# Optimization experiments

Measured on AMD Instinct MI355X. Metric: run time of the kernel, lower is better.

## Reference

```python
import jax, jax.numpy as jnp
import numpy as np

D_MODEL = 1024
NHEADS = 16
DK = D_MODEL // NHEADS  # 64
B, LQ, LK = 4, 1024, 1024


def setup_inputs() -> dict:
    key = jax.random.key(0)
    ks = jax.random.split(key, 5)
    q = jax.random.normal(ks[0], (B, LQ, NHEADS, DK), dtype=jnp.float32)
    k = jax.random.normal(ks[1], (B, LK, NHEADS, DK), dtype=jnp.float32)
    v = jax.random.normal(ks[2], (B, LK, NHEADS, DK), dtype=jnp.float32)
    # LazyLinear materializes with in_features = LK * NHEADS due to the
    # source bug (it projects the reshaped raw score tensor, not attn@V).
    fc_w = jax.random.normal(ks[3], (D_MODEL, LK * NHEADS), dtype=jnp.float32) * 0.02
    fc_b = jax.random.normal(ks[4], (D_MODEL,), dtype=jnp.float32) * 0.02
    return {"q": q, "k": k, "v": v, "fc_w": fc_w, "fc_b": fc_b}


def reference(q, k, v, fc_w, fc_b):
    # Raw scaled scores: [b, i, j, n]
    scores = jnp.einsum('bink,bjnk->bijn', q, k) / np.float32(np.sqrt(DK))
    # NOTE (faithful to source): the softmax(dim=1) and the attn@V einsum are
    # computed in the original but their result is discarded; the output is
    # built from the raw scores. v does not influence the output.
    b, i = scores.shape[0], scores.shape[1]
    out = scores.reshape(b, i, -1)            # [b, i, j*n]
    out = out @ fc_w.T + fc_b                 # Linear(j*n -> d_model)
    return out
```

## Files before the change

### kernel.cpp

```cpp
#include <hip/hip_runtime.h>
#include <hip/hip_bf16.h>


typedef unsigned short u16;
typedef unsigned int u32;
typedef __bf16 bf16x8 __attribute__((ext_vector_type(8)));
typedef float f32x4 __attribute__((ext_vector_type(4)));
typedef u16 u16x8 __attribute__((ext_vector_type(8)));

__device__ __forceinline__ u16 f2bf(float f) {
  union { float f; unsigned u; } in;
  in.f = f;
  unsigned u = in.u;
  u += 0x7fffu + ((u >> 16) & 1u);
  return (u16)(u >> 16);
}

__global__ __launch_bounds__(256) void prep(const float* __restrict__ k,
                                            const float* __restrict__ w,
                                            u16* __restrict__ Kt,
                                            u16* __restrict__ Wt) {
  __shared__ u16 lds[16 * 520];
  const int tid = threadIdx.x;
  const int bid = blockIdx.x;

  if (bid < 1024) {
    int jt = bid & 15, n = (bid >> 4) & 15, b = bid >> 8;
    auto l2 = reinterpret_cast<u16(*)[65]>(lds);
    const int j0 = jt * 64;
    float4 r[4];
#pragma unroll
    for (int it = 0; it < 4; ++it) {
      int idx = it * 256 + tid;
      int jj = idx >> 4;
      int c4 = idx & 15;
      r[it] = *reinterpret_cast<const float4*>(
          &k[(((size_t)b * 1024 + j0 + jj) * 16 + n) * 64 + c4 * 4]);
    }
#pragma unroll
    for (int it = 0; it < 4; ++it) {
      int idx = it * 256 + tid;
      int jj = idx >> 4;
      int c4 = idx & 15;
      l2[c4 * 4 + 0][jj] = f2bf(r[it].x);
      l2[c4 * 4 + 1][jj] = f2bf(r[it].y);
      l2[c4 * 4 + 2][jj] = f2bf(r[it].z);
      l2[c4 * 4 + 3][jj] = f2bf(r[it].w);
    }
    __syncthreads();
    ushort4 o[4];
#pragma unroll
    for (int it = 0; it < 4; ++it) {
      int idx = it * 256 + tid;
      int kk = idx >> 4;
      int c4 = idx & 15;
      o[it].x = l2[kk][c4 * 4 + 0]; o[it].y = l2[kk][c4 * 4 + 1];
      o[it].z = l2[kk][c4 * 4 + 2]; o[it].w = l2[kk][c4 * 4 + 3];
    }
#pragma unroll
    for (int it = 0; it < 4; ++it) {
      int idx = it * 256 + tid;
      int kk = idx >> 4;
      int c4 = idx & 15;
      *reinterpret_cast<ushort4*>(
          &Kt[((size_t)n * 256 + b * 64 + kk) * 1024 + j0 + c4 * 4]) = o[it];
    }
  } else {
    int e = bid - 1024;
    const int d = e >> 1;
    const int h = e & 1;
    u32* lds32 = reinterpret_cast<u32*>(lds);
    const float* src = w + (size_t)d * 16384 + h * 8192;

    float4 ra[4], rb[4];
    const int gbase = ((tid >> 2) << 3) + (tid & 3);
#pragma unroll
    for (int it = 0; it < 4; ++it) {
      int g1 = it * 512 + gbase;
      ra[it] = reinterpret_cast<const float4*>(src)[g1];
      rb[it] = reinterpret_cast<const float4*>(src)[g1 + 4];
    }
    const int n0 = (tid & 3) * 4;
#pragma unroll
    for (int it = 0; it < 4; ++it) {
      int a = (it * 512 + gbase) >> 2;
#pragma unroll
      for (int el = 0; el < 4; ++el) {
        float lo = (&ra[it].x)[el], hi = (&rb[it].x)[el];
        lds32[(n0 + el) * 260 + (a >> 1)] = (u32)f2bf(lo) | ((u32)f2bf(hi) << 16);
      }
    }
    __syncthreads();
    const int wv = tid >> 6, lane = tid & 63;
    u16x8 o[4];
#pragma unroll
    for (int s = 0; s < 4; ++s)
      o[s] = *reinterpret_cast<const u16x8*>(&lds[(4 * wv + s) * 520 + lane * 8]);
#pragma unroll
    for (int s = 0; s < 4; ++s) {
      int n = 4 * wv + s;
      *reinterpret_cast<u16x8*>(
          &Wt[(size_t)n * 1048576 + (size_t)d * 1024 + h * 512 + lane * 8]) = o[s];
    }
  }
}

template <int VM>
__device__ __forceinline__ void waitVm() {
  if constexpr (VM == 16) asm volatile("s_waitcnt vmcnt(16)" ::: "memory");
  else if constexpr (VM == 8) asm volatile("s_waitcnt vmcnt(8)" ::: "memory");
  else asm volatile("s_waitcnt vmcnt(0)" ::: "memory");
}

template <int TN_TILES, int STAGE>
__global__ __launch_bounds__(256, 1) void gemm_bt(const u16* __restrict__ Abase,
                                                  const u16* __restrict__ Bbase,
                                                  u16* __restrict__ CoutBf,
                                                  float* __restrict__ CoutF,
                                                  const float* __restrict__ bias,
                                                  const float* __restrict__ qsrc,
                                                  u16* __restrict__ qdst) {
  __shared__ u16 AB[4][2][128 * 64];
  const int tid = threadIdx.x;
  const int wid = tid >> 6;
  const int lane = tid & 63;
  const int batch = blockIdx.y;
  const int tm = blockIdx.x / TN_TILES;
  const int tn = blockIdx.x % TN_TILES;

  const u16* A = Abase + (size_t)batch * 1048576;
  const u16* B = Bbase + (size_t)batch * ((STAGE == 1) ? 262144 : 1048576);
  const int row0A = tm * 128, row0B = tn * 128;

  const int wr = wid >> 1;
  const int wc = wid & 1;
  const int laneRow = lane & 15;
  const int hi8 = (lane >> 4) * 8;
  const int swz = (lane & 7) * 8;

  f32x4 acc[4][4] = {};

  auto stage = [&](int tIdx) {
    const int kt = tIdx * 64;
    u16* lA = &AB[tIdx & 3][0][0];
    u16* lB = &AB[tIdx & 3][1][0];
#pragma unroll
    for (int i = 0; i < 4; ++i) {
      int p = i * 256 + tid;
      int r = p >> 3;
      int sc = ((p & 7) ^ (r & 7)) * 8;
      const u16* gA = A + (size_t)(row0A + r) * 1024 + kt + sc;
      const u16* gB = B + (size_t)(row0B + r) * 1024 + kt + sc;
      __builtin_amdgcn_global_load_lds(
          (const __attribute__((address_space(1))) void*)gA,
          (__attribute__((address_space(3))) void*)(lA + i * 2048 + wid * 512), 16, 0, 0);
      __builtin_amdgcn_global_load_lds(
          (const __attribute__((address_space(1))) void*)gB,
          (__attribute__((address_space(3))) void*)(lB + i * 2048 + wid * 512), 16, 0, 0);
    }
  };

  auto compute = [&](int tIdx) {
    const u16* At = &AB[tIdx & 3][0][0];
    const u16* Bt = &AB[tIdx & 3][1][0];
    bf16x8 af[2][4], bq[2][4];
#pragma unroll
    for (int kh = 0; kh < 2; ++kh) {
      int cs = (kh * 32 + hi8) ^ swz;
#pragma unroll
      for (int mi = 0; mi < 4; ++mi)
        af[kh][mi] = *reinterpret_cast<const bf16x8*>(
            &At[(wr * 64 + mi * 16 + laneRow) * 64 + cs]);
#pragma unroll
      for (int ni = 0; ni < 4; ++ni)
        bq[kh][ni] = *reinterpret_cast<const bf16x8*>(
            &Bt[(wc * 64 + ni * 16 + laneRow) * 64 + cs]);
    }
#pragma unroll
    for (int kh = 0; kh < 2; ++kh)
#pragma unroll
      for (int mi = 0; mi < 4; ++mi)
#pragma unroll
        for (int ni = 0; ni < 4; ++ni)
          acc[mi][ni] = __builtin_amdgcn_mfma_f32_16x16x32_bf16(
              af[kh][mi], bq[kh][ni], acc[mi][ni], 0, 0, 0);
  };

  stage(0); stage(1); stage(2);

  for (int t = 0; t < 13; ++t) {
    waitVm<16>();
    __builtin_amdgcn_s_barrier();
    stage(t + 3);
    compute(t);
  }
  waitVm<16>(); __builtin_amdgcn_s_barrier(); compute(13);
  waitVm<8>();  __builtin_amdgcn_s_barrier(); compute(14);
  waitVm<0>();  __builtin_amdgcn_s_barrier(); compute(15);

#pragma unroll
  for (int mi = 0; mi < 4; ++mi) {
#pragma unroll
    for (int ni = 0; ni < 4; ++ni) {
      int colg = tn * 128 + wc * 64 + ni * 16 + laneRow;
#pragma unroll
      for (int qq = 0; qq < 4; ++qq) {
        int rowg = tm * 128 + wr * 64 + mi * 16 + (lane >> 4) * 4 + qq;
        if (STAGE == 1) {
          size_t off = (size_t)(colg >> 6) * 1048576 + (size_t)rowg * 1024 +
                       (size_t)batch * 64 + (colg & 63);
          CoutBf[off] = f2bf(acc[mi][ni][qq]);
        } else {
          CoutF[(size_t)batch * 1048576 + (size_t)rowg * 1024 + colg] =
              acc[mi][ni][qq] * 0.125f + bias[colg];
        }
      }
    }
  }

  if (STAGE == 1) {
    const int cb = batch * 16 + blockIdx.x;
    const float4* src = reinterpret_cast<const float4*>(qsrc) + (size_t)cb * 4096;
    ushort4* dst = reinterpret_cast<ushort4*>(qdst) + (size_t)cb * 4096;
#pragma unroll
    for (int rnd = 0; rnd < 4; ++rnd) {
      float4 r[4];
#pragma unroll
      for (int i = 0; i < 4; ++i) r[i] = src[rnd * 1024 + i * 256 + tid];
#pragma unroll
      for (int i = 0; i < 4; ++i) {
        ushort4 o;
        o.x = f2bf(r[i].x); o.y = f2bf(r[i].y);
        o.z = f2bf(r[i].z); o.w = f2bf(r[i].w);
        dst[rnd * 1024 + i * 256 + tid] = o;
      }
    }
  }
}

extern "C" void kernel_launch(void* const* d_in, const int* in_sizes, int n_in,
                              void* d_out, int out_size, void* d_ws, size_t ws_size,
                              hipStream_t stream) {
  const float* q    = (const float*)d_in[0];
  const float* k    = (const float*)d_in[1];
  const float* fc_w = (const float*)d_in[3];
  const float* fc_b = (const float*)d_in[4];
  float* out = (float*)d_out;

  char* ws = (char*)d_ws;
  if (ws_size < 58720256) return;
  u16* Qb  = (u16*)(ws);
  u16* Kt  = (u16*)(ws + 8388608);
  u16* Wt  = (u16*)(ws + 16777216);
  u16* T2t = (u16*)(ws + 50331648);

  prep<<<3072, 256, 0, stream>>>(k, fc_w, Kt, Wt);
  gemm_bt<2, 1><<<dim3(16, 16), 256, 0, stream>>>(Wt, Kt, T2t, nullptr, nullptr, q, Qb);
  gemm_bt<8, 2><<<dim3(64, 4), 256, 0, stream>>>(Qb, T2t, nullptr, out, fc_b, nullptr, nullptr);
}
```

Baseline: 60.57 us.

## Fuse fc_w fp32-to-bf16 transpose into first GEMM's A-tile loading

Removes the separate pass that converted and transposed the 64MB fc_w into a bf16 Wt workspace. The first GEMM now reads fp32 weights directly, converts them in registers with packed bf16 conversion, and writes swizzled A tiles into LDS, using a double-buffered register-prefetch pipeline. The grid is reorganised so each block handles four heads, one per wave. This avoids writing and re-reading the 32MB bf16 weight copy, at the cost of more register pressure and a simpler two-stage pipeline in the first GEMM.

```diff
diff --git a/kernel.cpp b/kernel.cpp
--- a/kernel.cpp
+++ b/kernel.cpp
@@ -6,7 +6,6 @@
 typedef unsigned int u32;
 typedef __bf16 bf16x8 __attribute__((ext_vector_type(8)));
 typedef float f32x4 __attribute__((ext_vector_type(4)));
-typedef u16 u16x8 __attribute__((ext_vector_type(8)));
 
 __device__ __forceinline__ u16 f2bf(float f) {
   union { float f; unsigned u; } in;
@@ -16,91 +15,199 @@
   return (u16)(u >> 16);
 }
 
-__global__ __launch_bounds__(256) void prep(const float* __restrict__ k,
-                                            const float* __restrict__ w,
-                                            u16* __restrict__ Kt,
-                                            u16* __restrict__ Wt) {
-  __shared__ u16 lds[16 * 520];
+__device__ __forceinline__ u32 cvt_pk_bf16(float lo, float hi) {
+  u32 r;
+  asm("v_cvt_pk_bf16_f32 %0, %1, %2" : "=v"(r) : "v"(lo), "v"(hi));
+  return r;
+}
+
+__global__ __launch_bounds__(256) void prep_k(const float* __restrict__ k,
+                                              u16* __restrict__ Kt) {
+  __shared__ u16 lds[64][65];
   const int tid = threadIdx.x;
   const int bid = blockIdx.x;
-
-  if (bid < 1024) {
-    int jt = bid & 15, n = (bid >> 4) & 15, b = bid >> 8;
-    auto l2 = reinterpret_cast<u16(*)[65]>(lds);
-    const int j0 = jt * 64;
+  int jt = bid & 15, n = (bid >> 4) & 15, b = bid >> 8;
+  const int j0 = jt * 64;
+  float4 r[4];
+#pragma unroll
+  for (int it = 0; it < 4; ++it) {
+    int idx = it * 256 + tid;
+    int jj = idx >> 4;
+    int c4 = idx & 15;
+    r[it] = *reinterpret_cast<const float4*>(
+        &k[(((size_t)b * 1024 + j0 + jj) * 16 + n) * 64 + c4 * 4]);
+  }
+#pragma unroll
+  for (int it = 0; it < 4; ++it) {
+    int idx = it * 256 + tid;
+    int jj = idx >> 4;
+    int c4 = idx & 15;
+    lds[c4 * 4 + 0][jj] = f2bf(r[it].x);
+    lds[c4 * 4 + 1][jj] = f2bf(r[it].y);
+    lds[c4 * 4 + 2][jj] = f2bf(r[it].z);
+    lds[c4 * 4 + 3][jj] = f2bf(r[it].w);
+  }
+  __syncthreads();
+  ushort4 o[4];
+#pragma unroll
+  for (int it = 0; it < 4; ++it) {
+    int idx = it * 256 + tid;
+    int kk = idx >> 4;
+    int c4 = idx & 15;
+    o[it].x = lds[kk][c4 * 4 + 0]; o[it].y = lds[kk][c4 * 4 + 1];
+    o[it].z = lds[kk][c4 * 4 + 2]; o[it].w = lds[kk][c4 * 4 + 3];
+  }
+#pragma unroll
+  for (int it = 0; it < 4; ++it) {
+    int idx = it * 256 + tid;
+    int kk = idx >> 4;
+    int c4 = idx & 15;
+    *reinterpret_cast<ushort4*>(
+        &Kt[((size_t)n * 256 + b * 64 + kk) * 1024 + j0 + c4 * 4]) = o[it];
+  }
+}
+
+__global__ __launch_bounds__(256, 1) void gemm1f(const float* __restrict__ fw,
+                                                 const u16* __restrict__ Kt,
+                                                 u16* __restrict__ T2t,
+                                                 const float* __restrict__ qsrc,
+                                                 u16* __restrict__ qdst) {
+  __shared__ u16 LDS[65536];
+  u32* LDS32 = reinterpret_cast<u32*>(LDS);
+  const int tid = threadIdx.x;
+  const int w = tid >> 6;
+  const int lane = tid & 63;
+  const int nq = blockIdx.y;
+  const int tm = blockIdx.x >> 2;
+  const int tn = blockIdx.x & 3;
+  const int d0 = tm * 64;
+  const int laneRow = lane & 15;
+  const int hi = lane >> 4;
+
+  f32x4 acc[4][4] = {};
+  float4 ra[8], rb[8];
+
+  auto loadA = [&](int t) {
+    const int kt2 = t * 64;
+#pragma unroll
+    for (int i = 0; i < 8; ++i) {
+      int c = i * 256 + tid;
+      int dd = c >> 5;
+      int jp = c & 31;
+      const float* base = fw + (size_t)(d0 + dd) * 16384 + (size_t)(kt2 + 2 * jp) * 16 + nq * 4;
+      ra[i] = *reinterpret_cast<const float4*>(base);
+      rb[i] = *reinterpret_cast<const float4*>(base + 16);
+    }
+  };
+
+  auto writeA = [&](int buf) {
+    const int wb = buf * 8192;
+#pragma unroll
+    for (int i = 0; i < 8; ++i) {
+      int c = i * 256 + tid;
+      int dd = c >> 5;
+      int jp = c & 31;
+      int jps = jp ^ ((dd & 7) << 2);
+      int a = wb + dd * 32 + jps;
+      LDS32[a + 0 * 2048] = cvt_pk_bf16(ra[i].x, rb[i].x);
+      LDS32[a + 1 * 2048] = cvt_pk_bf16(ra[i].y, rb[i].y);
+      LDS32[a + 2 * 2048] = cvt_pk_bf16(ra[i].z, rb[i].z);
+      LDS32[a + 3 * 2048] = cvt_pk_bf16(ra[i].w, rb[i].w);
+    }
+  };
+
+  auto stageB = [&](int t, int buf) {
+    const int kt2 = t * 64;
+#pragma unroll
+    for (int i = 0; i < 8; ++i) {
+      int p = i * 256 + tid;
+      int np_ = p >> 9;
+      int r = (p >> 3) & 63;
+      int cb2 = p & 7;
+      int scb = cb2 ^ (r & 7);
+      const u16* src = Kt + ((size_t)(nq * 4 + np_) * 256 + tn * 64 + r) * 1024 + kt2 + scb * 8;
+      u16* dst = &LDS[32768 + buf * 16384 + p * 8];
+      __builtin_amdgcn_global_load_lds(
+          (const __attribute__((address_space(1))) void*)src,
+          (__attribute__((address_space(3))) void*)dst, 16, 0, 0);
+    }
+  };
+
+  auto compute = [&](int buf) {
+    const int Ab = buf * 16384 + w * 4096;
+    const int Bb = 32768 + buf * 16384 + w * 4096;
+    bf16x8 af[2][4], bq[2][4];
+#pragma unroll
+    for (int kh = 0; kh < 2; ++kh) {
+      int g = kh * 4 + hi;
+#pragma unroll
+      for (int mi = 0; mi < 4; ++mi) {
+        int dd = mi * 16 + laneRow;
+        af[kh][mi] = *reinterpret_cast<const bf16x8*>(&LDS[Ab + dd * 64 + (g ^ (dd & 7)) * 8]);
+      }
+#pragma unroll
+      for (int ni = 0; ni < 4; ++ni) {
+        int rr = ni * 16 + laneRow;
+        bq[kh][ni] = *reinterpret_cast<const bf16x8*>(&LDS[Bb + rr * 64 + (g ^ (rr & 7)) * 8]);
+      }
+    }
+#pragma unroll
+    for (int kh = 0; kh < 2; ++kh)
+#pragma unroll
+      for (int mi = 0; mi < 4; ++mi)
+#pragma unroll
+        for (int ni = 0; ni < 4; ++ni)
+          acc[mi][ni] = __builtin_amdgcn_mfma_f32_16x16x32_bf16(
+              af[kh][mi], bq[kh][ni], acc[mi][ni], 0, 0, 0);
+  };
+
+  loadA(0);
+  stageB(0, 0);
+  writeA(0);
+  __syncthreads();
+
+  for (int t = 0; t < 16; ++t) {
+    const int cur = t & 1;
+    if (t < 15) {
+      stageB(t + 1, cur ^ 1);
+      loadA(t + 1);
+    }
+    compute(cur);
+    if (t < 15) {
+      writeA(cur ^ 1);
+      __syncthreads();
+    }
+  }
+
+  const int n = nq * 4 + w;
+#pragma unroll
+  for (int mi = 0; mi < 4; ++mi) {
+#pragma unroll
+    for (int ni = 0; ni < 4; ++ni) {
+      int colg = ni * 16 + laneRow;
+#pragma unroll
+      for (int qq = 0; qq < 4; ++qq) {
+        int rowg = mi * 16 + hi * 4 + qq;
+        T2t[(size_t)tn * 1048576 + (size_t)(d0 + rowg) * 1024 + n * 64 + colg] =
+            f2bf(acc[mi][ni][qq]);
+      }
+    }
+  }
+
+  const int cb = nq * 64 + blockIdx.x;
+  const float4* src = reinterpret_cast<const float4*>(qsrc) + (size_t)cb * 4096;
+  ushort4* dst = reinterpret_cast<ushort4*>(qdst) + (size_t)cb * 4096;
+#pragma unroll
+  for (int rnd = 0; rnd < 4; ++rnd) {
     float4 r[4];
 #pragma unroll
-    for (int it = 0; it < 4; ++it) {
-      int idx = it * 256 + tid;
-      int jj = idx >> 4;
-      int c4 = idx & 15;
-      r[it] = *reinterpret_cast<const float4*>(
-          &k[(((size_t)b * 1024 + j0 + jj) * 16 + n) * 64 + c4 * 4]);
-    }
-#pragma unroll
-    for (int it = 0; it < 4; ++it) {
-      int idx = it * 256 + tid;
-      int jj = idx >> 4;
-      int c4 = idx & 15;
-      l2[c4 * 4 + 0][jj] = f2bf(r[it].x);
-      l2[c4 * 4 + 1][jj] = f2bf(r[it].y);
-      l2[c4 * 4 + 2][jj] = f2bf(r[it].z);
-      l2[c4 * 4 + 3][jj] = f2bf(r[it].w);
-    }
-    __syncthreads();
-    ushort4 o[4];
-#pragma unroll
-    for (int it = 0; it < 4; ++it) {
-      int idx = it * 256 + tid;
-      int kk = idx >> 4;
-      int c4 = idx & 15;
-      o[it].x = l2[kk][c4 * 4 + 0]; o[it].y = l2[kk][c4 * 4 + 1];
-      o[it].z = l2[kk][c4 * 4 + 2]; o[it].w = l2[kk][c4 * 4 + 3];
-    }
-#pragma unroll
-    for (int it = 0; it < 4; ++it) {
-      int idx = it * 256 + tid;
-      int kk = idx >> 4;
-      int c4 = idx & 15;
-      *reinterpret_cast<ushort4*>(
-          &Kt[((size_t)n * 256 + b * 64 + kk) * 1024 + j0 + c4 * 4]) = o[it];
-    }
-  } else {
-    int e = bid - 1024;
-    const int d = e >> 1;
-    const int h = e & 1;
-    u32* lds32 = reinterpret_cast<u32*>(lds);
-    const float* src = w + (size_t)d * 16384 + h * 8192;
-
-    float4 ra[4], rb[4];
-    const int gbase = ((tid >> 2) << 3) + (tid & 3);
-#pragma unroll
-    for (int it = 0; it < 4; ++it) {
-      int g1 = it * 512 + gbase;
-      ra[it] = reinterpret_cast<const float4*>(src)[g1];
-      rb[it] = reinterpret_cast<const float4*>(src)[g1 + 4];
-    }
-    const int n0 = (tid & 3) * 4;
-#pragma unroll
-    for (int it = 0; it < 4; ++it) {
-      int a = (it * 512 + gbase) >> 2;
-#pragma unroll
-      for (int el = 0; el < 4; ++el) {
-        float lo = (&ra[it].x)[el], hi = (&rb[it].x)[el];
-        lds32[(n0 + el) * 260 + (a >> 1)] = (u32)f2bf(lo) | ((u32)f2bf(hi) << 16);
-      }
-    }
-    __syncthreads();
-    const int wv = tid >> 6, lane = tid & 63;
-    u16x8 o[4];
-#pragma unroll
-    for (int s = 0; s < 4; ++s)
-      o[s] = *reinterpret_cast<const u16x8*>(&lds[(4 * wv + s) * 520 + lane * 8]);
-#pragma unroll
-    for (int s = 0; s < 4; ++s) {
-      int n = 4 * wv + s;
-      *reinterpret_cast<u16x8*>(
-          &Wt[(size_t)n * 1048576 + (size_t)d * 1024 + h * 512 + lane * 8]) = o[s];
+    for (int i = 0; i < 4; ++i) r[i] = src[rnd * 1024 + i * 256 + tid];
+#pragma unroll
+    for (int i = 0; i < 4; ++i) {
+      ushort4 o;
+      o.x = f2bf(r[i].x); o.y = f2bf(r[i].y);
+      o.z = f2bf(r[i].z); o.w = f2bf(r[i].w);
+      dst[rnd * 1024 + i * 256 + tid] = o;
     }
   }
 }
@@ -112,24 +219,20 @@
   else asm volatile("s_waitcnt vmcnt(0)" ::: "memory");
 }
 
-template <int TN_TILES, int STAGE>
-__global__ __launch_bounds__(256, 1) void gemm_bt(const u16* __restrict__ Abase,
-                                                  const u16* __restrict__ Bbase,
-                                                  u16* __restrict__ CoutBf,
-                                                  float* __restrict__ CoutF,
-                                                  const float* __restrict__ bias,
-                                                  const float* __restrict__ qsrc,
-                                                  u16* __restrict__ qdst) {
+__global__ __launch_bounds__(256, 1) void gemm2(const u16* __restrict__ Abase,
+                                                const u16* __restrict__ Bbase,
+                                                float* __restrict__ CoutF,
+                                                const float* __restrict__ bias) {
   __shared__ u16 AB[4][2][128 * 64];
   const int tid = threadIdx.x;
   const int wid = tid >> 6;
   const int lane = tid & 63;
   const int batch = blockIdx.y;
-  const int tm = blockIdx.x / TN_TILES;
-  const int tn = blockIdx.x % TN_TILES;
+  const int tm = blockIdx.x >> 3;
+  const int tn = blockIdx.x & 7;
 
   const u16* A = Abase + (size_t)batch * 1048576;
-  const u16* B = Bbase + (size_t)batch * ((STAGE == 1) ? 262144 : 1048576);
+  const u16* B = Bbase + (size_t)batch * 1048576;
   const int row0A = tm * 128, row0B = tn * 128;
 
   const int wr = wid >> 1;
@@ -187,7 +290,6 @@
   };
 
   stage(0); stage(1); stage(2);
-
   for (int t = 0; t < 13; ++t) {
     waitVm<16>();
     __builtin_amdgcn_s_barrier();
@@ -206,33 +308,8 @@
 #pragma unroll
       for (int qq = 0; qq < 4; ++qq) {
         int rowg = tm * 128 + wr * 64 + mi * 16 + (lane >> 4) * 4 + qq;
-        if (STAGE == 1) {
-          size_t off = (size_t)(colg >> 6) * 1048576 + (size_t)rowg * 1024 +
-                       (size_t)batch * 64 + (colg & 63);
-          CoutBf[off] = f2bf(acc[mi][ni][qq]);
-        } else {
-          CoutF[(size_t)batch * 1048576 + (size_t)rowg * 1024 + colg] =
-              acc[mi][ni][qq] * 0.125f + bias[colg];
-        }
-      }
-    }
-  }
-
-  if (STAGE == 1) {
-    const int cb = batch * 16 + blockIdx.x;
-    const float4* src = reinterpret_cast<const float4*>(qsrc) + (size_t)cb * 4096;
-    ushort4* dst = reinterpret_cast<ushort4*>(qdst) + (size_t)cb * 4096;
-#pragma unroll
-    for (int rnd = 0; rnd < 4; ++rnd) {
-      float4 r[4];
-#pragma unroll
-      for (int i = 0; i < 4; ++i) r[i] = src[rnd * 1024 + i * 256 + tid];
-#pragma unroll
-      for (int i = 0; i < 4; ++i) {
-        ushort4 o;
-        o.x = f2bf(r[i].x); o.y = f2bf(r[i].y);
-        o.z = f2bf(r[i].z); o.w = f2bf(r[i].w);
-        dst[rnd * 1024 + i * 256 + tid] = o;
+        CoutF[(size_t)batch * 1048576 + (size_t)rowg * 1024 + colg] =
+            acc[mi][ni][qq] * 0.125f + bias[colg];
       }
     }
   }
@@ -251,10 +328,9 @@
   if (ws_size < 58720256) return;
   u16* Qb  = (u16*)(ws);
   u16* Kt  = (u16*)(ws + 8388608);
-  u16* Wt  = (u16*)(ws + 16777216);
   u16* T2t = (u16*)(ws + 50331648);
 
-  prep<<<3072, 256, 0, stream>>>(k, fc_w, Kt, Wt);
-  gemm_bt<2, 1><<<dim3(16, 16), 256, 0, stream>>>(Wt, Kt, T2t, nullptr, nullptr, q, Qb);
-  gemm_bt<8, 2><<<dim3(64, 4), 256, 0, stream>>>(Qb, T2t, nullptr, out, fc_b, nullptr, nullptr);
-}
+  prep_k<<<1024, 256, 0, stream>>>(k, Kt);
+  gemm1f<<<dim3(64, 4), 256, 0, stream>>>(fc_w, Kt, T2t, q, Qb);
+  gemm2<<<dim3(64, 4), 256, 0, stream>>>(Qb, T2t, out, fc_b);
+}
```

New measurement: 100.7 us. 1.66x slower.
